# Kernel optimization log

Hardware: AMD Instinct MI355X
Metric: run time of the kernel (lower is better)

## Reference

```python
import jax, jax.numpy as jnp
import numpy as np

HIDDEN = 128
NUM_FILTERS = 128
NUM_RBF = 50
NUM_LAYERS = 3
MAX_Z = 100
CUTOFF_LO, CUTOFF_HI = 0.0, 5.0
N_ATOMS = 10000
N_EDGES = 320000


def _xavier(k, shape):
    fan_out, fan_in = shape[-2], shape[-1]
    a = (6.0 / (fan_in + fan_out)) ** 0.5
    return jax.random.uniform(k, shape, jnp.float32, -a, a)


def setup_inputs() -> dict:
    key = jax.random.key(0)
    ks = jax.random.split(key, 16)
    start = float(np.exp(-CUTOFF_HI + CUTOFF_LO))  # ExpNormalSmearing start value
    L = NUM_LAYERS
    return {
        "z": jax.random.randint(ks[0], (N_ATOMS,), 0, MAX_Z),
        "edge_index": jax.random.randint(ks[1], (2, N_EDGES), 0, N_ATOMS),
        "edge_weight": jax.random.uniform(ks[2], (N_EDGES,), jnp.float32, 0.0, CUTOFF_HI),
        "emb_table": jax.random.normal(ks[3], (MAX_Z, HIDDEN), jnp.float32),
        "means": jnp.linspace(start, 1.0, NUM_RBF, dtype=jnp.float32),
        "betas": jnp.full((NUM_RBF,), (2.0 / NUM_RBF * (1.0 - start)) ** -2, dtype=jnp.float32),
        "ne_proj_w": _xavier(ks[4], (HIDDEN, NUM_RBF)),
        "ne_proj_b": jnp.zeros((HIDDEN,), jnp.float32),
        "ne_comb_w": _xavier(ks[5], (HIDDEN, 2 * HIDDEN)),
        "ne_comb_b": jnp.zeros((HIDDEN,), jnp.float32),
        "mlp_w0": _xavier(ks[6], (L, NUM_FILTERS, NUM_RBF)),
        "mlp_b0": jnp.zeros((L, NUM_FILTERS), jnp.float32),
        "mlp_w1": _xavier(ks[7], (L, NUM_FILTERS, NUM_FILTERS)),
        "mlp_b1": jnp.zeros((L, NUM_FILTERS), jnp.float32),
        "lin1_w": _xavier(ks[8], (L, NUM_FILTERS, HIDDEN)),
        "lin2_w": _xavier(ks[9], (L, HIDDEN, NUM_FILTERS)),
        "lin2_b": jnp.zeros((L, HIDDEN), jnp.float32),
        "lin_w": _xavier(ks[10], (L, HIDDEN, HIDDEN)),
        "lin_b": jnp.zeros((L, HIDDEN), jnp.float32),
    }


def _cosine_cutoff(d):
    c = 0.5 * (jnp.cos(d * (jnp.pi / CUTOFF_HI)) + 1.0)
    return jnp.where(d < CUTOFF_HI, c, 0.0)


def reference(z, edge_index, edge_weight, emb_table, means, betas,
              ne_proj_w, ne_proj_b, ne_comb_w, ne_comb_b,
              mlp_w0, mlp_b0, mlp_w1, mlp_b1, lin1_w, lin2_w, lin2_b, lin_w, lin_b):
    n_atoms = z.shape[0]
    src, dst = edge_index[0], edge_index[1]
    alpha = 5.0 / (CUTOFF_HI - CUTOFF_LO)
    C = _cosine_cutoff(edge_weight)  # [E]
    # ExpNormalSmearing (includes cutoff factor)
    rbf = jnp.exp(-betas * (jnp.exp(alpha * (CUTOFF_LO - edge_weight))[:, None] - means) ** 2)
    edge_attr = C[:, None] * rbf  # [E, NUM_RBF]

    x = emb_table[z]  # [N, H]

    # NeighborEmbedding (self loops masked out, as in the original)
    mask = (src != dst)[:, None]
    W = (edge_attr @ ne_proj_w.T + ne_proj_b) * C[:, None]
    W = jnp.where(mask, W, 0.0)
    agg = jax.ops.segment_sum(W * emb_table[z][dst], src, num_segments=n_atoms)
    x = jnp.concatenate([x, agg], axis=1) @ ne_comb_w.T + ne_comb_b

    def layer(xc, p):
        w0, b0, w1, b1, l1w, l2w, l2b, lw, lb = p
        # filter network: MLP(edge_attr) * cutoff
        Wf = (jax.nn.silu(edge_attr @ w0.T + b0) @ w1.T + b1) * C[:, None]  # [E, F]
        h = xc @ l1w.T                                   # lin1 (no bias) [N, F]
        a = jax.ops.segment_sum(Wf * h[dst], src, num_segments=n_atoms)  # scatter-add
        h = jax.nn.silu(a @ l2w.T + l2b)                 # lin2 + act
        h = h @ lw.T + lb                                # final linear
        return xc + h, None

    x, _ = jax.lax.scan(layer, x, (mlp_w0, mlp_b0, mlp_w1, mlp_b1, lin1_w, lin2_w, lin2_b, lin_w, lin_b))
    return x
```

## Files before the change

### kernel.cpp

```cpp
#include <hip/hip_runtime.h>
#include <hip/hip_bf16.h>

#define NATOMS 10000
#define NEDGES 320000
#define H 128
#define NRBF 50
#define NELEM (NATOMS * H)
#define NT 4096

typedef unsigned short u16;
typedef unsigned int u32;
typedef __attribute__((ext_vector_type(8))) short short8;
typedef __attribute__((ext_vector_type(4))) float float4v;

__device__ __forceinline__ float bfu(u16 u) { return __uint_as_float(((u32)u) << 16); }
__device__ __forceinline__ u16 bf16r(float v) {
    u32 u = __float_as_uint(v);
    return (u16)((u + 0x7FFFu + ((u >> 16) & 1u)) >> 16);
}
__device__ __forceinline__ float ldf(const void* p, int i, int bf) {
    return bf ? bfu(((const u16*)p)[i]) : ((const float*)p)[i];
}
__device__ __forceinline__ float silu_f(float v) { return v / (1.f + __expf(-v)); }
__device__ __forceinline__ int bfflag(const void* means) {
    return ((((const u32*)means)[24] >> 16) == 0x3F80u) ? 1 : 0;
}

__global__ __launch_bounds__(256) void k_embed(const int* __restrict__ z, const void* emb,
                                               const void* means,
                                               float* __restrict__ x0, u16* __restrict__ xh,
                                               int* __restrict__ degz,
                                               float* __restrict__ zb) {
    int bf = bfflag(means);
    int i = blockIdx.x * 256 + threadIdx.x;
    if (i < 20480) degz[i] = 0;
    if (i < NELEM / 4) ((float4*)zb)[i] = make_float4(0.f, 0.f, 0.f, 0.f);
    if (i < NELEM) {
        int n = i >> 7, f = i & 127;
        float v = ldf(emb, z[n] * H + f, bf);
        x0[i] = v;
        xh[i] = bf16r(v);
    }
}

__device__ __forceinline__ void stage_w16(const void* W, int woff, int wstride,
                                          u16* sW, int tid, int nthr, int bf) {
    u32* sW32 = (u32*)sW;
    if (bf) {
        const u32* W32 = (const u32*)W;
        for (int i = tid; i < 128 * 64; i += nthr) {
            int f2 = i >> 6, kk = i & 63;
            sW32[f2 * 68 + kk] = W32[((woff + f2 * wstride) >> 1) + kk];
        }
    } else {
        const float2* Wf = (const float2*)W;
        for (int i = tid; i < 128 * 64; i += nthr) {
            int f2 = i >> 6, kk = i & 63;
            float2 v = Wf[((woff + f2 * wstride) >> 1) + kk];
            sW32[f2 * 68 + kk] = (u32)bf16r(v.x) | ((u32)bf16r(v.y) << 16);
        }
    }
}

__global__ __launch_bounds__(256) void k_mfma_lin(const float* in,
                                                  const void* W2, int w2off,
                                                  const void* B2, int b2off,
                                                  const void* Wl, int wloff,
                                                  const void* Bl, int bloff,
                                                  const void* W1n, int w1noff,
                                                  float* x, u16* __restrict__ hb,
                                                  const void* means,
                                                  float* zrw, void* outp) {
    __shared__ u16 sW2[128 * 136];
    __shared__ u16 sWl[128 * 136];
    __shared__ u16 sW1[128 * 136];
    __shared__ u16 sA[4][16 * 136];
    __shared__ float sB2v[128], sBlv[128];
    int tid = threadIdx.x;
    int bf = bfflag(means);
    stage_w16(W2, w2off, H, sW2, tid, 256, bf);
    stage_w16(Wl, wloff, H, sWl, tid, 256, bf);
    if (W1n) stage_w16(W1n, w1noff, H, sW1, tid, 256, bf);
    if (tid < 128) {
        sB2v[tid] = ldf(B2, b2off + tid, bf);
        sBlv[tid] = ldf(Bl, bloff + tid, bf);
    }
    __syncthreads();
    int w = tid >> 6, lane = tid & 63;
    int quad = lane >> 4, l16 = lane & 15;
    u16* myA = sA[w];
    u32* myA32 = (u32*)myA;
    for (int tile = blockIdx.x * 4 + w; tile < NATOMS / 16; tile += gridDim.x * 4) {
        int abase = tile * 16;
        const float2* in2 = (const float2*)in + (size_t)abase * 64;
        #pragma unroll 4
        for (int j = 0; j < 16; ++j) {
            float2 v = in2[j * 64 + lane];
            myA32[j * 68 + lane] = (u32)bf16r(v.x) | ((u32)bf16r(v.y) << 16);
        }
        __asm__ volatile("s_waitcnt lgkmcnt(0)" ::: "memory");
        if (zrw) {
            float2* z2 = (float2*)zrw + (size_t)abase * 64;
            #pragma unroll 4
            for (int j = 0; j < 16; ++j) z2[j * 64 + lane] = make_float2(0.f, 0.f);
        }
        short8 af0 = *(const short8*)&myA[l16 * 136 +   0 + quad * 8];
        short8 af1 = *(const short8*)&myA[l16 * 136 +  32 + quad * 8];
        short8 af2 = *(const short8*)&myA[l16 * 136 +  64 + quad * 8];
        short8 af3 = *(const short8*)&myA[l16 * 136 +  96 + quad * 8];
        #pragma unroll 1
        for (int nt = 0; nt < 8; ++nt) {
            const u16* wrow = &sW2[(nt * 16 + l16) * 136];
            short8 b0 = *(const short8*)&wrow[0  + quad * 8];
            short8 b1 = *(const short8*)&wrow[32 + quad * 8];
            short8 b2 = *(const short8*)&wrow[64 + quad * 8];
            short8 b3 = *(const short8*)&wrow[96 + quad * 8];
            float4v acc = {0.f, 0.f, 0.f, 0.f};
            acc = __builtin_amdgcn_mfma_f32_16x16x32_bf16(af0, b0, acc, 0, 0, 0);
            acc = __builtin_amdgcn_mfma_f32_16x16x32_bf16(af1, b1, acc, 0, 0, 0);
            acc = __builtin_amdgcn_mfma_f32_16x16x32_bf16(af2, b2, acc, 0, 0, 0);
            acc = __builtin_amdgcn_mfma_f32_16x16x32_bf16(af3, b3, acc, 0, 0, 0);
            int col = nt * 16 + l16;
            float bias = sB2v[col];
            myA[(quad * 4 + 0) * 136 + col] = bf16r(silu_f(acc[0] + bias));
            myA[(quad * 4 + 1) * 136 + col] = bf16r(silu_f(acc[1] + bias));
            myA[(quad * 4 + 2) * 136 + col] = bf16r(silu_f(acc[2] + bias));
            myA[(quad * 4 + 3) * 136 + col] = bf16r(silu_f(acc[3] + bias));
        }
        __asm__ volatile("s_waitcnt lgkmcnt(0)" ::: "memory");
        short8 t0 = *(const short8*)&myA[l16 * 136 +   0 + quad * 8];
        short8 t1 = *(const short8*)&myA[l16 * 136 +  32 + quad * 8];
        short8 t2 = *(const short8*)&myA[l16 * 136 +  64 + quad * 8];
        short8 t3 = *(const short8*)&myA[l16 * 136 +  96 + quad * 8];
        #pragma unroll 1
        for (int nt = 0; nt < 8; ++nt) {
            const u16* wrow = &sWl[(nt * 16 + l16) * 136];
            short8 b0 = *(const short8*)&wrow[0  + quad * 8];
            short8 b1 = *(const short8*)&wrow[32 + quad * 8];
            short8 b2 = *(const short8*)&wrow[64 + quad * 8];
            short8 b3 = *(const short8*)&wrow[96 + quad * 8];
            int col = nt * 16 + l16;
            float bias = sBlv[col];
            float4v acc;
            acc[0] = x[(size_t)(abase + quad * 4 + 0) * H + col] + bias;
            acc[1] = x[(size_t)(abase + quad * 4 + 1) * H + col] + bias;
            acc[2] = x[(size_t)(abase + quad * 4 + 2) * H + col] + bias;
            acc[3] = x[(size_t)(abase + quad * 4 + 3) * H + col] + bias;
            acc = __builtin_amdgcn_mfma_f32_16x16x32_bf16(t0, b0, acc, 0, 0, 0);
            acc = __builtin_amdgcn_mfma_f32_16x16x32_bf16(t1, b1, acc, 0, 0, 0);
            acc = __builtin_amdgcn_mfma_f32_16x16x32_bf16(t2, b2, acc, 0, 0, 0);
            acc = __builtin_amdgcn_mfma_f32_16x16x32_bf16(t3, b3, acc, 0, 0, 0);
            #pragma unroll
            for (int r = 0; r < 4; ++r) {
                size_t idx = (size_t)(abase + quad * 4 + r) * H + col;
                x[idx] = acc[r];
                myA[(quad * 4 + r) * 136 + col] = bf16r(acc[r]);
                if (outp) {
                    if (bf) ((u16*)outp)[idx] = bf16r(acc[r]);
                    else    ((float*)outp)[idx] = acc[r];
                }
            }
        }
        if (W1n) {
            __asm__ volatile("s_waitcnt lgkmcnt(0)" ::: "memory");
            short8 h0 = *(const short8*)&myA[l16 * 136 +   0 + quad * 8];
            short8 h1 = *(const short8*)&myA[l16 * 136 +  32 + quad * 8];
            short8 h2 = *(const short8*)&myA[l16 * 136 +  64 + quad * 8];
            short8 h3 = *(const short8*)&myA[l16 * 136 +  96 + quad * 8];
            #pragma unroll 1
            for (int nt = 0; nt < 8; ++nt) {
                const u16* wrow = &sW1[(nt * 16 + l16) * 136];
                short8 b0 = *(const short8*)&wrow[0  + quad * 8];
                short8 b1 = *(const short8*)&wrow[32 + quad * 8];
                short8 b2 = *(const short8*)&wrow[64 + quad * 8];
                short8 b3 = *(const short8*)&wrow[96 + quad * 8];
                float4v acc = {0.f, 0.f, 0.f, 0.f};
                acc = __builtin_amdgcn_mfma_f32_16x16x32_bf16(h0, b0, acc, 0, 0, 0);
                acc = __builtin_amdgcn_mfma_f32_16x16x32_bf16(h1, b1, acc, 0, 0, 0);
                acc = __builtin_amdgcn_mfma_f32_16x16x32_bf16(h2, b2, acc, 0, 0, 0);
                acc = __builtin_amdgcn_mfma_f32_16x16x32_bf16(h3, b3, acc, 0, 0, 0);
                int col = nt * 16 + l16;
                hb[(size_t)(abase + quad * 4 + 0) * H + col] = bf16r(acc[0]);
                hb[(size_t)(abase + quad * 4 + 1) * H + col] = bf16r(acc[1]);
                hb[(size_t)(abase + quad * 4 + 2) * H + col] = bf16r(acc[2]);
                hb[(size_t)(abase + quad * 4 + 3) * H + col] = bf16r(acc[3]);
            }
        }
    }
}

__global__ __launch_bounds__(256) void k_mfma_comb(const float* in0, float* in1,
                                                   const void* W, const void* B,
                                                   const void* W1,
                                                   float* x, u16* __restrict__ hb,
                                                   const void* means) {
    __shared__ u16 sWa[128 * 136];
    __shared__ u16 sWb[128 * 136];
    __shared__ u16 sW1[128 * 136];
    __shared__ u16 sA[4][16 * 136];
    __shared__ float sBv[128];
    int tid = threadIdx.x;
    int bf = bfflag(means);
    stage_w16(W, 0,   256, sWa, tid, 256, bf);
    stage_w16(W, 128, 256, sWb, tid, 256, bf);
    stage_w16(W1, 0, H, sW1, tid, 256, bf);
    if (tid < 128) sBv[tid] = ldf(B, tid, bf);
    __syncthreads();
    int w = tid >> 6, lane = tid & 63;
    int quad = lane >> 4, l16 = lane & 15;
    u16* myA = sA[w];
    u32* myA32 = (u32*)myA;
    for (int tile = blockIdx.x * 4 + w; tile < NATOMS / 16; tile += gridDim.x * 4) {
        int abase = tile * 16;
        const float2* i0 = (const float2*)in0 + (size_t)abase * 64;
        const float2* i1 = (const float2*)in1 + (size_t)abase * 64;
        #pragma unroll 4
        for (int j = 0; j < 16; ++j) {
            float2 v = i0[j * 64 + lane];
            myA32[j * 68 + lane] = (u32)bf16r(v.x) | ((u32)bf16r(v.y) << 16);
        }
        __asm__ volatile("s_waitcnt lgkmcnt(0)" ::: "memory");
        short8 af0 = *(const short8*)&myA[l16 * 136 +   0 + quad * 8];
        short8 af1 = *(const short8*)&myA[l16 * 136 +  32 + quad * 8];
        short8 af2 = *(const short8*)&myA[l16 * 136 +  64 + quad * 8];
        short8 af3 = *(const short8*)&myA[l16 * 136 +  96 + quad * 8];
        #pragma unroll 4
        for (int j = 0; j < 16; ++j) {
            float2 v = i1[j * 64 + lane];
            myA32[j * 68 + lane] = (u32)bf16r(v.x) | ((u32)bf16r(v.y) << 16);
        }
        __asm__ volatile("s_waitcnt lgkmcnt(0)" ::: "memory");
        {
            float2* z2 = (float2*)in1 + (size_t)abase * 64;
            #pragma unroll 4
            for (int j = 0; j < 16; ++j) z2[j * 64 + lane] = make_float2(0.f, 0.f);
        }
        short8 ag0 = *(const short8*)&myA[l16 * 136 +   0 + quad * 8];
        short8 ag1 = *(const short8*)&myA[l16 * 136 +  32 + quad * 8];
        short8 ag2 = *(const short8*)&myA[l16 * 136 +  64 + quad * 8];
        short8 ag3 = *(const short8*)&myA[l16 * 136 +  96 + quad * 8];
        #pragma unroll 1
        for (int nt = 0; nt < 8; ++nt) {
            const u16* wra = &sWa[(nt * 16 + l16) * 136];
            const u16* wrb = &sWb[(nt * 16 + l16) * 136];
            int col = nt * 16 + l16;
            float bias = sBv[col];
            float4v acc = {bias, bias, bias, bias};
            acc = __builtin_amdgcn_mfma_f32_16x16x32_bf16(af0, *(const short8*)&wra[0  + quad * 8], acc, 0, 0, 0);
            acc = __builtin_amdgcn_mfma_f32_16x16x32_bf16(af1, *(const short8*)&wra[32 + quad * 8], acc, 0, 0, 0);
            acc = __builtin_amdgcn_mfma_f32_16x16x32_bf16(af2, *(const short8*)&wra[64 + quad * 8], acc, 0, 0, 0);
            acc = __builtin_amdgcn_mfma_f32_16x16x32_bf16(af3, *(const short8*)&wra[96 + quad * 8], acc, 0, 0, 0);
            acc = __builtin_amdgcn_mfma_f32_16x16x32_bf16(ag0, *(const short8*)&wrb[0  + quad * 8], acc, 0, 0, 0);
            acc = __builtin_amdgcn_mfma_f32_16x16x32_bf16(ag1, *(const short8*)&wrb[32 + quad * 8], acc, 0, 0, 0);
            acc = __builtin_amdgcn_mfma_f32_16x16x32_bf16(ag2, *(const short8*)&wrb[64 + quad * 8], acc, 0, 0, 0);
            acc = __builtin_amdgcn_mfma_f32_16x16x32_bf16(ag3, *(const short8*)&wrb[96 + quad * 8], acc, 0, 0, 0);
            #pragma unroll
            for (int r = 0; r < 4; ++r) {
                x[(size_t)(abase + quad * 4 + r) * H + col] = acc[r];
                myA[(quad * 4 + r) * 136 + col] = bf16r(acc[r]);
            }
        }
        __asm__ volatile("s_waitcnt lgkmcnt(0)" ::: "memory");
        short8 h0 = *(const short8*)&myA[l16 * 136 +   0 + quad * 8];
        short8 h1 = *(const short8*)&myA[l16 * 136 +  32 + quad * 8];
        short8 h2 = *(const short8*)&myA[l16 * 136 +  64 + quad * 8];
        short8 h3 = *(const short8*)&myA[l16 * 136 +  96 + quad * 8];
        #pragma unroll 1
        for (int nt = 0; nt < 8; ++nt) {
            const u16* wrow = &sW1[(nt * 16 + l16) * 136];
            short8 b0 = *(const short8*)&wrow[0  + quad * 8];
            short8 b1 = *(const short8*)&wrow[32 + quad * 8];
            short8 b2 = *(const short8*)&wrow[64 + quad * 8];
            short8 b3 = *(const short8*)&wrow[96 + quad * 8];
            float4v acc = {0.f, 0.f, 0.f, 0.f};
            acc = __builtin_amdgcn_mfma_f32_16x16x32_bf16(h0, b0, acc, 0, 0, 0);
            acc = __builtin_amdgcn_mfma_f32_16x16x32_bf16(h1, b1, acc, 0, 0, 0);
            acc = __builtin_amdgcn_mfma_f32_16x16x32_bf16(h2, b2, acc, 0, 0, 0);
            acc = __builtin_amdgcn_mfma_f32_16x16x32_bf16(h3, b3, acc, 0, 0, 0);
            int col = nt * 16 + l16;
            hb[(size_t)(abase + quad * 4 + 0) * H + col] = bf16r(acc[0]);
            hb[(size_t)(abase + quad * 4 + 1) * H + col] = bf16r(acc[1]);
            hb[(size_t)(abase + quad * 4 + 2) * H + col] = bf16r(acc[2]);
            hb[(size_t)(abase + quad * 4 + 3) * H + col] = bf16r(acc[3]);
        }
    }
}

__global__ __launch_bounds__(1024) void k_ft4(const void* means, const void* betas,
                                              const void* W0s, const void* B0s,
                                              const void* W1s, const void* B1s,
                                              const void* Wne, const void* Bne,
                                              u16* __restrict__ ftT,
                                              u16* __restrict__ Tne) {
    __shared__ float sW0[H * 53];
    __shared__ u16 sW1b[128 * 136];
    __shared__ u16 sA16[16 * 136];
    __shared__ float sR[16][56];
    __shared__ float sM[NRBF], sBe[NRBF], sB1v[128], sC[16];
    int tid = threadIdx.x;
    int bf = bfflag(means);
    int t = blockIdx.x >> 8;
    int bb = blockIdx.x & 255;
    int ne = (t == 3);
    const void* W0 = ne ? Wne : W0s;
    int w0off = ne ? 0 : t * H * NRBF;
    u16* T = ne ? Tne : (ftT + (size_t)t * NT * H);
    if (!ne) stage_w16(W1s, t * H * H, H, sW1b, tid, 1024, bf);
    for (int i = tid; i < H * NRBF; i += 1024) {
        int f2 = i / NRBF, k = i - f2 * NRBF;
        sW0[f2 * 53 + k] = ldf(W0, w0off + i, bf);
    }
    if (tid < NRBF) { sM[tid] = ldf(means, tid, bf); sBe[tid] = ldf(betas, tid, bf); }
    if (tid < 128) sB1v[tid] = ne ? 0.f : ldf(B1s, t * H + tid, bf);
    __syncthreads();
    int g = tid >> 7, f = tid & 127;
    float b0r = ne ? ldf(Bne, f, bf) : ldf(B0s, t * H + f, bf);
    int base = bb * 16;
    int n0 = base + 2 * g, n1 = n0 + 1;
    float wv0 = (float)n0 * (5.0f / (NT - 1));
    float wv1 = (float)n1 * (5.0f / (NT - 1));
    if (f < NRBF) {
        float tt = expf(-wv0) - sM[f];
        sR[2 * g][f] = expf(-sBe[f] * tt * tt);
    } else if (f >= 64 && f < 64 + NRBF) {
        float tt = expf(-wv1) - sM[f - 64];
        sR[2 * g + 1][f - 64] = expf(-sBe[f - 64] * tt * tt);
    }
    __syncthreads();
    float c0 = 0.5f * (cosf(wv0 * 0.62831853071795864f) + 1.f); if (!(wv0 < 5.f)) c0 = 0.f;
    float c1 = 0.5f * (cosf(wv1 * 0.62831853071795864f) + 1.f); if (!(wv1 < 5.f)) c1 = 0.f;
    if (f == 0) { sC[2 * g] = c0; sC[2 * g + 1] = c1; }
    float s0 = 0.f, s1 = 0.f;
    #pragma unroll
    for (int k = 0; k < NRBF; ++k) {
        float wk = sW0[f * 53 + k];
        s0 = fmaf(wk, sR[2 * g][k], s0);
        s1 = fmaf(wk, sR[2 * g + 1][k], s1);
    }
    if (ne) {
        T[(size_t)n0 * H + f] = bf16r(fmaf(c0, s0, b0r) * c0);
        T[(size_t)n1 * H + f] = bf16r(fmaf(c1, s1, b0r) * c1);
        return;
    }
    sA16[(2 * g) * 136 + f]     = bf16r(silu_f(fmaf(c0, s0, b0r)));
    sA16[(2 * g + 1) * 136 + f] = bf16r(silu_f(fmaf(c1, s1, b0r)));
    __syncthreads();
    int w = tid >> 6;
    if (w < 8) {
        int lane = tid & 63;
        int quad = lane >> 4, l16 = lane & 15;
        short8 a0 = *(const short8*)&sA16[l16 * 136 +   0 + quad * 8];
        short8 a1 = *(const short8*)&sA16[l16 * 136 +  32 + quad * 8];
        short8 a2 = *(const short8*)&sA16[l16 * 136 +  64 + quad * 8];
        short8 a3 = *(const short8*)&sA16[l16 * 136 +  96 + quad * 8];
        const u16* wrow = &sW1b[(w * 16 + l16) * 136];
        short8 b0 = *(const short8*)&wrow[0  + quad * 8];
        short8 b1 = *(const short8*)&wrow[32 + quad * 8];
        short8 b2 = *(const short8*)&wrow[64 + quad * 8];
        short8 b3 = *(const short8*)&wrow[96 + quad * 8];
        float4v acc = {0.f, 0.f, 0.f, 0.f};
        acc = __builtin_amdgcn_mfma_f32_16x16x32_bf16(a0, b0, acc, 0, 0, 0);
        acc = __builtin_amdgcn_mfma_f32_16x16x32_bf16(a1, b1, acc, 0, 0, 0);
        acc = __builtin_amdgcn_mfma_f32_16x16x32_bf16(a2, b2, acc, 0, 0, 0);
        acc = __builtin_amdgcn_mfma_f32_16x16x32_bf16(a3, b3, acc, 0, 0, 0);
        int col = w * 16 + l16;
        float bias = sB1v[col];
        #pragma unroll
        for (int r = 0; r < 4; ++r) {
            int row = quad * 4 + r;
            T[(size_t)(base + row) * H + col] = bf16r((acc[r] + bias) * sC[row]);
        }
    }
}

__global__ __launch_bounds__(256) void k_hist(const int* __restrict__ src, int* __restrict__ deg) {
    int e = blockIdx.x * 256 + threadIdx.x;
    if (e < NEDGES) atomicAdd(&deg[src[e]], 1);
}

__global__ __launch_bounds__(1024) void k_scan(const int* __restrict__ deg, int* __restrict__ rs) {
    __shared__ int buf[1024];
    __shared__ int carry;
    int tid = threadIdx.x;
    if (tid == 0) carry = 0;
    __syncthreads();
    for (int c = 0; c < 10; ++c) {
        int i = c * 1024 + tid;
        int v = (i < NATOMS) ? deg[i] : 0;
        buf[tid] = v;
        __syncthreads();
        for (int off = 1; off < 1024; off <<= 1) {
            int t = (tid >= off) ? buf[tid - off] : 0;
            __syncthreads();
            buf[tid] += t;
            __syncthreads();
        }
        int base = carry;
        if (i < NATOMS) rs[i] = base + buf[tid] - v;
        __syncthreads();
        if (tid == 0) carry = base + buf[1023];
        __syncthreads();
    }
}

__global__ __launch_bounds__(256) void k_scatter_perm(const int* __restrict__ src,
                                                      const int* __restrict__ dst,
                                                      const void* ew, const void* means,
                                                      const int* __restrict__ rs,
                                                      int* __restrict__ cnt,
                                                      int* __restrict__ srcs,
                                                      int* __restrict__ dsts,
                                                      float* __restrict__ ews) {
    int bf = bfflag(means);
    int e = blockIdx.x * 256 + threadIdx.x;
    if (e < NEDGES) {
        int s = src[e];
        int p = rs[s] + atomicAdd(&cnt[s], 1);
        srcs[p] = s;
        dsts[p] = dst[e];
        ews[p] = ldf(ew, e, bf);
    }
}

#define ELOAD(i) \
    int s##i = srcs[e + i], d##i = dsts[e + i]; \
    float u##i = ews[e + i] * ((float)(NT - 1) / 5.0f); \
    int ix##i = min((int)u##i, NT - 2); float fr##i = u##i - (float)ix##i; \
    u32 ta##i = Tb[ix##i * 64 + lane], tb##i = Tb[ix##i * 64 + 64 + lane]; \
    u32 h##i = vh[d##i * 64 + lane];
#define EVAL(i) \
    float vx##i = fmaf(fr##i, bfu((u16)(tb##i & 0xffff)) - bfu((u16)(ta##i & 0xffff)), bfu((u16)(ta##i & 0xffff))) * bfu((u16)(h##i & 0xffff)); \
    float vy##i = fmaf(fr##i, bfu((u16)(tb##i >> 16))    - bfu((u16)(ta##i >> 16)),    bfu((u16)(ta##i >> 16)))    * bfu((u16)(h##i >> 16));
#define EACC(i) \
    if (!(mask_self && s##i == d##i)) { \
        if (s##i != cur) { \
            if (cur >= 0) { atomicAdd(&acc[cur * H + 2 * lane], rx); atomicAdd(&acc[cur * H + 2 * lane + 1], ry); } \
            cur = s##i; rx = 0.f; ry = 0.f; \
        } \
        rx += vx##i; ry += vy##i; \
    }

__global__ __launch_bounds__(256) void k_edge_apply4(const int* __restrict__ srcs,
                                                     const int* __restrict__ dsts,
                                                     const float* __restrict__ ews,
                                                     const u32* __restrict__ Tb,
                                                     const u32* __restrict__ vh,
                                                     float* __restrict__ acc,
                                                     int mask_self) {
    int tid = threadIdx.x;
    int g = tid >> 6;
    int lane = tid & 63;
    int gid = blockIdx.x * 4 + g;
    int r0 = gid * 40;
    int cur = -1;
    float rx = 0.f, ry = 0.f;
    for (int e = r0; e < r0 + 40; e += 8) {
        ELOAD(0) ELOAD(1) ELOAD(2) ELOAD(3) ELOAD(4) ELOAD(5) ELOAD(6) ELOAD(7)
        EVAL(0) EVAL(1) EVAL(2) EVAL(3) EVAL(4) EVAL(5) EVAL(6) EVAL(7)
        EACC(0) EACC(1) EACC(2) EACC(3) EACC(4) EACC(5) EACC(6) EACC(7)
    }
    if (cur >= 0) {
        atomicAdd(&acc[cur * H + 2 * lane], rx);
        atomicAdd(&acc[cur * H + 2 * lane + 1], ry);
    }
}

extern "C" void kernel_launch(void* const* d_in, const int* in_sizes, int n_in,
                              void* d_out, int out_size, void* d_ws, size_t ws_size,
                              hipStream_t stream) {
    const int* z  = (const int*)d_in[0];
    const int* ei = (const int*)d_in[1];
    const void* ew        = d_in[2];
    const void* emb       = d_in[3];
    const void* means     = d_in[4];
    const void* betas     = d_in[5];
    const void* ne_proj_w = d_in[6];
    const void* ne_proj_b = d_in[7];
    const void* ne_comb_w = d_in[8];
    const void* ne_comb_b = d_in[9];
    const void* mlp_w0    = d_in[10];
    const void* mlp_b0    = d_in[11];
    const void* mlp_w1    = d_in[12];
    const void* mlp_b1    = d_in[13];
    const void* lin1_w    = d_in[14];
    const void* lin2_w    = d_in[15];
    const void* lin2_b    = d_in[16];
    const void* lin_w     = d_in[17];
    const void* lin_b     = d_in[18];

    const int* srcp = ei;
    const int* dstp = ei + NEDGES;

    float* buf0 = (float*)d_ws;
    float* buf1 = buf0 + NELEM;
    float* x    = buf1 + NELEM;
    int*   deg  = (int*)(x + NELEM);
    int*   cnt  = deg + 10240;
    int*   rs   = cnt + 10240;
    int*   srcs = rs + 10240;
    int*   dsts = srcs + NEDGES;
    float* ews  = (float*)(dsts + NEDGES);
    u16*   Tb   = (u16*)(ews + NEDGES);
    u16*   hb   = Tb + NT * H;
    u16*   ftT  = hb + NELEM;

    const int gElem = (NELEM + 255) / 256;
    const int gEdge = (NEDGES + 255) / 256;

    k_embed<<<gElem, 256, 0, stream>>>(z, emb, means, buf0, hb, deg, buf1);

    k_hist<<<gEdge, 256, 0, stream>>>(srcp, deg);
    k_scan<<<1, 1024, 0, stream>>>(deg, rs);
    k_scatter_perm<<<gEdge, 256, 0, stream>>>(srcp, dstp, ew, means, rs, cnt,
                                              srcs, dsts, ews);

    k_ft4<<<1024, 1024, 0, stream>>>(means, betas, mlp_w0, mlp_b0, mlp_w1, mlp_b1,
                                     ne_proj_w, ne_proj_b, ftT, Tb);

    k_edge_apply4<<<2000, 256, 0, stream>>>(srcs, dsts, ews, (const u32*)Tb,
                                            (const u32*)hb, buf1, 1);
    k_mfma_comb<<<157, 256, 0, stream>>>(buf0, buf1, ne_comb_w, ne_comb_b,
                                         lin1_w, x, hb, means);

    for (int L = 0; L < 3; ++L) {
        k_edge_apply4<<<2000, 256, 0, stream>>>(srcs, dsts, ews,
                                                (const u32*)(ftT + (size_t)L * NT * H),
                                                (const u32*)hb, buf1, 0);
        k_mfma_lin<<<157, 256, 0, stream>>>(buf1, lin2_w, L * H * H, lin2_b, L * H,
                                            lin_w, L * H * H, lin_b, L * H,
                                            (L < 2) ? lin1_w : nullptr, (L + 1) * H * H,
                                            x, hb, means,
                                            (L < 2) ? buf1 : nullptr,
                                            (L == 2) ? d_out : nullptr);
    }
}
```

Before: 366.3 us.

## Pack src/dst into one word, prescale edge weights, and use a shuffle-based scan

Replaces the single-block chunked Hillis-Steele scan (many __syncthreads per chunk) with a per-thread serial scan of 10 elements, wavefront shuffle scans and a small shared array of wave sums. Packs src (14 bits) and dst into one 32-bit word per sorted edge and stores edge weights already scaled to table-index units. This cuts the per-edge index loads in the four edge-apply passes and removes one multiply per edge. The packing depends on atom ids fitting in 14 bits, which holds for 10000 atoms.

```diff
diff --git a/kernel.cpp b/kernel.cpp
--- a/kernel.cpp
+++ b/kernel.cpp
@@ -379,27 +379,41 @@
 }
 
 __global__ __launch_bounds__(1024) void k_scan(const int* __restrict__ deg, int* __restrict__ rs) {
-    __shared__ int buf[1024];
-    __shared__ int carry;
+    __shared__ int wsum[16];
     int tid = threadIdx.x;
-    if (tid == 0) carry = 0;
-    __syncthreads();
-    for (int c = 0; c < 10; ++c) {
-        int i = c * 1024 + tid;
-        int v = (i < NATOMS) ? deg[i] : 0;
-        buf[tid] = v;
-        __syncthreads();
-        for (int off = 1; off < 1024; off <<= 1) {
-            int t = (tid >= off) ? buf[tid - off] : 0;
-            __syncthreads();
-            buf[tid] += t;
-            __syncthreads();
-        }
-        int base = carry;
-        if (i < NATOMS) rs[i] = base + buf[tid] - v;
-        __syncthreads();
-        if (tid == 0) carry = base + buf[1023];
-        __syncthreads();
+    int lane = tid & 63, w = tid >> 6;
+    int d[10];
+    int tot = 0;
+    int base_i = tid * 10;
+    if (tid < 1000) {
+        #pragma unroll
+        for (int j = 0; j < 10; ++j) d[j] = deg[base_i + j];
+        #pragma unroll
+        for (int j = 0; j < 10; ++j) { int v = d[j]; d[j] = tot; tot += v; }
+    }
+    int inc = tot;
+    #pragma unroll
+    for (int off = 1; off < 64; off <<= 1) {
+        int n = __shfl_up(inc, off, 64);
+        if (lane >= off) inc += n;
+    }
+    if (lane == 63) wsum[w] = inc;
+    __syncthreads();
+    if (w == 0) {
+        int v = (lane < 16) ? wsum[lane] : 0;
+        int vinc = v;
+        #pragma unroll
+        for (int off = 1; off < 16; off <<= 1) {
+            int n = __shfl_up(vinc, off, 64);
+            if (lane >= off) vinc += n;
+        }
+        if (lane < 16) wsum[lane] = vinc - v;
+    }
+    __syncthreads();
+    if (tid < 1000) {
+        int base = wsum[w] + (inc - tot);
+        #pragma unroll
+        for (int j = 0; j < 10; ++j) rs[base_i + j] = base + d[j];
     }
 }
 
@@ -408,23 +422,22 @@
                                                       const void* ew, const void* means,
                                                       const int* __restrict__ rs,
                                                       int* __restrict__ cnt,
-                                                      int* __restrict__ srcs,
-                                                      int* __restrict__ dsts,
+                                                      u32* __restrict__ sds,
                                                       float* __restrict__ ews) {
     int bf = bfflag(means);
     int e = blockIdx.x * 256 + threadIdx.x;
     if (e < NEDGES) {
         int s = src[e];
         int p = rs[s] + atomicAdd(&cnt[s], 1);
-        srcs[p] = s;
-        dsts[p] = dst[e];
-        ews[p] = ldf(ew, e, bf);
+        sds[p] = (u32)s | ((u32)dst[e] << 14);
+        ews[p] = ldf(ew, e, bf) * ((float)(NT - 1) / 5.0f);
     }
 }
 
 #define ELOAD(i) \
-    int s##i = srcs[e + i], d##i = dsts[e + i]; \
-    float u##i = ews[e + i] * ((float)(NT - 1) / 5.0f); \
+    u32 sd##i = sds[e + i]; \
+    int s##i = (int)(sd##i & 16383u), d##i = (int)(sd##i >> 14); \
+    float u##i = ews[e + i]; \
     int ix##i = min((int)u##i, NT - 2); float fr##i = u##i - (float)ix##i; \
     u32 ta##i = Tb[ix##i * 64 + lane], tb##i = Tb[ix##i * 64 + 64 + lane]; \
     u32 h##i = vh[d##i * 64 + lane];
@@ -440,8 +453,7 @@
         rx += vx##i; ry += vy##i; \
     }
 
-__global__ __launch_bounds__(256) void k_edge_apply4(const int* __restrict__ srcs,
-                                                     const int* __restrict__ dsts,
+__global__ __launch_bounds__(256) void k_edge_apply4(const u32* __restrict__ sds,
                                                      const float* __restrict__ ews,
                                                      const u32* __restrict__ Tb,
                                                      const u32* __restrict__ vh,
@@ -497,9 +509,8 @@
     int*   deg  = (int*)(x + NELEM);
     int*   cnt  = deg + 10240;
     int*   rs   = cnt + 10240;
-    int*   srcs = rs + 10240;
-    int*   dsts = srcs + NEDGES;
-    float* ews  = (float*)(dsts + NEDGES);
+    u32*   sds  = (u32*)(rs + 10240);
+    float* ews  = (float*)(sds + NEDGES);
     u16*   Tb   = (u16*)(ews + NEDGES);
     u16*   hb   = Tb + NT * H;
     u16*   ftT  = hb + NELEM;
@@ -512,18 +523,18 @@
     k_hist<<<gEdge, 256, 0, stream>>>(srcp, deg);
     k_scan<<<1, 1024, 0, stream>>>(deg, rs);
     k_scatter_perm<<<gEdge, 256, 0, stream>>>(srcp, dstp, ew, means, rs, cnt,
-                                              srcs, dsts, ews);
+                                              sds, ews);
 
     k_ft4<<<1024, 1024, 0, stream>>>(means, betas, mlp_w0, mlp_b0, mlp_w1, mlp_b1,
                                      ne_proj_w, ne_proj_b, ftT, Tb);
 
-    k_edge_apply4<<<2000, 256, 0, stream>>>(srcs, dsts, ews, (const u32*)Tb,
+    k_edge_apply4<<<2000, 256, 0, stream>>>(sds, ews, (const u32*)Tb,
                                             (const u32*)hb, buf1, 1);
     k_mfma_comb<<<157, 256, 0, stream>>>(buf0, buf1, ne_comb_w, ne_comb_b,
                                          lin1_w, x, hb, means);
 
     for (int L = 0; L < 3; ++L) {
-        k_edge_apply4<<<2000, 256, 0, stream>>>(srcs, dsts, ews,
+        k_edge_apply4<<<2000, 256, 0, stream>>>(sds, ews,
                                                 (const u32*)(ftT + (size_t)L * NT * H),
                                                 (const u32*)hb, buf1, 0);
         k_mfma_lin<<<157, 256, 0, stream>>>(buf1, lin2_w, L * H * H, lin2_b, L * H,
```

Result: faster. 344.3 us (-6.0%).
